# Optimization experiments

Measured on AMD Instinct MI355X. Metric: run time of the kernel, lower is better.

Reference implementation:

```python
import jax, jax.numpy as jnp
import numpy as np

N_NODES = 100000
N_EDGES = 1600000
N_GRAPHS = 128
IN_FEATS = 128
OUT_FEATS = 64


def setup_inputs() -> dict:
    key = jax.random.key(0)
    k1, k2, k3, k4, k5, k6 = jax.random.split(key, 6)
    features = jax.random.normal(k1, (N_NODES, IN_FEATS), jnp.float32)
    src = jax.random.randint(k2, (N_EDGES,), 0, N_NODES, dtype=jnp.int32)
    dst = jax.random.randint(k3, (N_EDGES,), 0, N_NODES, dtype=jnp.int32)
    graph_ids = jnp.sort(jax.random.randint(k4, (N_NODES,), 0, N_GRAPHS, dtype=jnp.int32))
    # Xavier-uniform init as in DGL GraphConv
    lim1 = float(np.sqrt(6.0 / (IN_FEATS + IN_FEATS)))
    lim2 = float(np.sqrt(6.0 / (IN_FEATS + OUT_FEATS)))
    W1 = jax.random.uniform(k5, (IN_FEATS, IN_FEATS), jnp.float32, -lim1, lim1)
    W2 = jax.random.uniform(k6, (IN_FEATS, OUT_FEATS), jnp.float32, -lim2, lim2)
    b1 = jnp.zeros((IN_FEATS,), jnp.float32)
    b2 = jnp.zeros((OUT_FEATS,), jnp.float32)
    return {"features": features, "W1": W1, "b1": b1, "W2": W2, "b2": b2,
            "src": src, "dst": dst, "graph_ids": graph_ids, "num_graphs": N_GRAPHS}


def _graph_conv(x, W, b, src, dst, n_nodes):
    # DGL GraphConv, norm='both': D_dst^{-1/2} A D_src^{-1/2} X W + b
    ones = jnp.ones(src.shape, x.dtype)
    deg_out = jax.ops.segment_sum(ones, src, num_segments=n_nodes)
    deg_in = jax.ops.segment_sum(ones, dst, num_segments=n_nodes)
    norm_src = jax.lax.rsqrt(jnp.maximum(deg_out, 1.0))  # [N]
    norm_dst = jax.lax.rsqrt(jnp.maximum(deg_in, 1.0))   # [N]
    h = (x * norm_src[:, None]) @ W                       # dense transform first
    agg = jax.ops.segment_sum(h[src], dst, num_segments=n_nodes)  # spmm-style scatter-add
    return agg * norm_dst[:, None] + b


def reference(features, W1, b1, W2, b2, src, dst, graph_ids, num_graphs):
    n = features.shape[0]
    h = jax.nn.relu(_graph_conv(features, W1, b1, src, dst, n))
    h = jax.nn.relu(_graph_conv(h, W2, b2, src, dst, n))
    # dgl.mean_nodes: per-graph mean over nodes
    sums = jax.ops.segment_sum(h, graph_ids, num_segments=num_graphs)
    counts = jax.ops.segment_sum(jnp.ones((n, 1), h.dtype), graph_ids, num_segments=num_graphs)
    return sums / jnp.maximum(counts, 1.0)
```

## Files before the change

### kernel.cpp

```cpp
#include <hip/hip_runtime.h>
#include <hip/hip_bf16.h>


#define NPP_SHIFT 9
#define NPP 512
#define MAXP 256
#define NB 512
#define CAPP 10240

typedef __attribute__((ext_vector_type(8))) short frag8;
typedef __attribute__((ext_vector_type(4))) float f32x4;
typedef __attribute__((ext_vector_type(2))) float v2f;

__launch_bounds__(256)
__global__ void buildC(const int* __restrict__ src, const int* __restrict__ dst,
                       int E, int P, int* __restrict__ cur,
                       int2* __restrict__ ebuf_dst, int* __restrict__ deg,
                       const int* __restrict__ gids, int N, int G,
                       int* __restrict__ gcnt) {
    __shared__ int h[MAXP], bs[MAXP], hg[MAXP];
    int tid = threadIdx.x;
    for (int i = tid; i < MAXP; i += 256) { h[i] = 0; hg[i] = 0; }
    __syncthreads();
    int per_block = (E + NB - 1) / NB;
    int e0 = blockIdx.x * per_block;
    int e1 = min(e0 + per_block, E);
    for (int e = e0 + tid; e < e1; e += 256) {
        atomicAdd(&h[dst[e] >> NPP_SHIFT], 1);
        atomicAdd(&deg[src[e]], 1);
    }
    int npb = (N + NB - 1) / NB;
    int n0 = blockIdx.x * npb;
    int n1 = min(n0 + npb, N);
    for (int i = n0 + tid; i < n1; i += 256) atomicAdd(&hg[gids[i]], 1);
    __syncthreads();
    for (int p = tid; p < P; p += 256) {
        int c = h[p];
        bs[p] = c ? atomicAdd(&cur[p], c) : 0;
        h[p] = 0;
    }
    for (int i = tid; i < G; i += 256)
        if (hg[i]) atomicAdd(&gcnt[i], hg[i]);
    __syncthreads();
    for (int e = e0 + tid; e < e1; e += 256) {
        int d = dst[e];
        int s = src[e];
        int p = d >> NPP_SHIFT;
        int lp = atomicAdd(&h[p], 1);
        ebuf_dst[(size_t)p * CAPP + bs[p] + lp] = make_int2(d, s);
    }
}

__launch_bounds__(512)
__global__ void passD2(const int2* __restrict__ ebuf_dst, const int* __restrict__ cur,
                       int* __restrict__ row_start, int* __restrict__ csr_src,
                       int N, int E, int P) {
    __shared__ int hd[NPP], sc[NPP];
    int tid = threadIdx.x;
    int p = blockIdx.x;
    sc[tid] = (tid < P) ? cur[tid] : 0;
    __syncthreads();
    for (int off = 1; off < 512; off <<= 1) {
        int t = (tid >= off) ? sc[tid - off] : 0;
        __syncthreads();
        sc[tid] += t;
        __syncthreads();
    }
    int gbase = (p > 0) ? sc[p - 1] : 0;
    __syncthreads();
    int node_lo = p << NPP_SHIFT;
    int nl = min(NPP, N - node_lo);
    hd[tid] = 0;
    __syncthreads();
    int ndst = cur[p];
    size_t base_d = (size_t)p * CAPP;
    for (int i = tid; i < ndst; i += 512)
        atomicAdd(&hd[ebuf_dst[base_d + i].x - node_lo], 1);
    __syncthreads();
    int myh = hd[tid];
    sc[tid] = myh;
    __syncthreads();
    for (int off = 1; off < 512; off <<= 1) {
        int t = (tid >= off) ? sc[tid - off] : 0;
        __syncthreads();
        sc[tid] += t;
        __syncthreads();
    }
    int row0 = gbase + sc[tid] - myh;
    if (tid < nl) row_start[node_lo + tid] = row0;
    if (p == P - 1 && tid == 0) row_start[N] = E;
    __syncthreads();
    hd[tid] = row0;
    __syncthreads();
    for (int i = tid; i < ndst; i += 512) {
        int2 r = ebuf_dst[base_d + i];
        int pos = atomicAdd(&hd[r.x - node_lo], 1);
        csr_src[pos] = r.y;
    }
}

template <int COLS, bool BF16IN, bool PERM, bool FP8OUT>
__launch_bounds__(256)
__global__ void gemm_mfma(const void* __restrict__ xin, const float* __restrict__ w,
                          const int* __restrict__ deg,
                          void* __restrict__ out, int n) {
    constexpr int NT = COLS / 16;
    __shared__ short wlds[4 * NT * 64 * 8];
    const int tid = threadIdx.x;
    for (int i = tid; i < 128 * COLS / 4; i += 256) {
        int k = (i * 4) / COLS;
        int n0 = (i * 4) % COLS;
        float4 wv;
        if constexpr (PERM) {
            int ksrc = 64 * ((k >> 2) & 1) + 16 * (k & 3) + (k >> 3);
            wv = *reinterpret_cast<const float4*>(w + (size_t)ksrc * COLS + n0);
        } else {
            wv = reinterpret_cast<const float4*>(w)[i];
        }
        int c = k >> 5, q = (k >> 3) & 3, j = k & 7;
        float vals[4] = {wv.x, wv.y, wv.z, wv.w};
#pragma unroll
        for (int u = 0; u < 4; ++u) {
            int nn = n0 + u;
            int t = nn >> 4;
            int ln = (q << 4) | (nn & 15);
            union { __hip_bfloat16 b; short s; } cv;
            cv.b = __float2bfloat16(vals[u]);
            wlds[(((c * NT + t) << 6) | ln) * 8 + j] = cv.s;
        }
    }
    __syncthreads();

    const int lane = tid & 63;
    const int wid = tid >> 6;
    const int m = lane & 15;
    const int q = lane >> 4;
    const int ntiles = (n + 15) >> 4;
    const frag8* wfr = reinterpret_cast<const frag8*>(wlds);

    for (int wt = blockIdx.x * 4 + wid; wt < ntiles; wt += gridDim.x * 4) {
        const int row = (wt << 4) + m;
        frag8 af[4];
        if (row < n) {
            if constexpr (BF16IN) {
                const frag8* xp = reinterpret_cast<const frag8*>(
                    (const __hip_bfloat16*)xin + (size_t)row * 128);
#pragma unroll
                for (int c = 0; c < 4; ++c) af[c] = xp[c * 4 + q];
            } else {
                const float* xp = (const float*)xin + (size_t)row * 128;
                float nm = rsqrtf((float)max(deg[row], 1));
#pragma unroll
                for (int c = 0; c < 4; ++c) {
                    int base = c * 32 + q * 8;
                    float4 v0 = *reinterpret_cast<const float4*>(xp + base);
                    float4 v1 = *reinterpret_cast<const float4*>(xp + base + 4);
                    union { frag8 f; short s[8]; } a;
                    union { __hip_bfloat16 b; short s; } cv;
                    cv.b = __float2bfloat16(v0.x * nm); a.s[0] = cv.s;
                    cv.b = __float2bfloat16(v0.y * nm); a.s[1] = cv.s;
                    cv.b = __float2bfloat16(v0.z * nm); a.s[2] = cv.s;
                    cv.b = __float2bfloat16(v0.w * nm); a.s[3] = cv.s;
                    cv.b = __float2bfloat16(v1.x * nm); a.s[4] = cv.s;
                    cv.b = __float2bfloat16(v1.y * nm); a.s[5] = cv.s;
                    cv.b = __float2bfloat16(v1.z * nm); a.s[6] = cv.s;
                    cv.b = __float2bfloat16(v1.w * nm); a.s[7] = cv.s;
                    af[c] = a.f;
                }
            }
        } else {
#pragma unroll
            for (int c = 0; c < 4; ++c) af[c] = frag8{0, 0, 0, 0, 0, 0, 0, 0};
        }
        f32x4 acc[NT] = {};
#pragma unroll
        for (int c = 0; c < 4; ++c)
#pragma unroll
            for (int t = 0; t < NT; ++t)
                acc[t] = __builtin_amdgcn_mfma_f32_16x16x32_bf16(
                    af[c], wfr[(c * NT + t) * 64 + lane], acc[t], 0, 0, 0);
#pragma unroll
        for (int r = 0; r < 4; ++r) {
            int grow = (wt << 4) + q * 4 + r;
            if (grow < n) {
                if constexpr (FP8OUT && COLS == 128) {
                    uint w0 = 0, w1 = 0;
                    w0 = (uint)__builtin_amdgcn_cvt_pk_fp8_f32(acc[0][r], acc[1][r], (int)w0, false);
                    w0 = (uint)__builtin_amdgcn_cvt_pk_fp8_f32(acc[2][r], acc[3][r], (int)w0, true);
                    w1 = (uint)__builtin_amdgcn_cvt_pk_fp8_f32(acc[4][r], acc[5][r], (int)w1, false);
                    w1 = (uint)__builtin_amdgcn_cvt_pk_fp8_f32(acc[6][r], acc[7][r], (int)w1, true);
                    reinterpret_cast<uint2*>(out)[(size_t)grow * 16 + m] = make_uint2(w0, w1);
                } else if constexpr (FP8OUT) {
                    uint w0 = 0;
                    w0 = (uint)__builtin_amdgcn_cvt_pk_fp8_f32(acc[0][r], acc[1][r], (int)w0, false);
                    w0 = (uint)__builtin_amdgcn_cvt_pk_fp8_f32(acc[2][r], acc[3][r], (int)w0, true);
                    reinterpret_cast<uint*>(out)[(size_t)grow * 16 + m] = w0;
                } else {
                    __hip_bfloat16* ob = reinterpret_cast<__hip_bfloat16*>(out);
#pragma unroll
                    for (int t = 0; t < NT; ++t)
                        ob[(size_t)grow * COLS + t * 16 + m] = __float2bfloat16(acc[t][r]);
                }
            }
        }
    }
}

__launch_bounds__(256)
__global__ void spmm1_kernel(const uint2* __restrict__ h1,
                             const int* __restrict__ row_start,
                             const int* __restrict__ csr_src,
                             const float* __restrict__ b1,
                             const int* __restrict__ deg,
                             uint4* __restrict__ x2n, int n) {
    int wv = (blockIdx.x * blockDim.x + threadIdx.x) >> 6;
    int lane = threadIdx.x & 63;
    int r0 = wv * 2;
    if (r0 >= n) return;
    int a = lane >> 4;
    int s = lane & 15;
    int e0[2], e1[2];
#pragma unroll
    for (int r = 0; r < 2; ++r) {
        int rr = min(r0 + r, n - 1);
        e0[r] = row_start[rr];
        e1[r] = row_start[rr + 1];
        if (r0 + r >= n) e1[r] = e0[r];
    }
    v2f acc[2][4] = {};
    int nb = max((e1[0] - e0[0] + 15) >> 4, (e1[1] - e0[1] + 15) >> 4);
    for (int b = 0; b < nb; ++b) {
        uint2 v[2][4];
#pragma unroll
        for (int r = 0; r < 2; ++r) {
            int base = e0[r] + b * 16;
            if (base + 16 <= e1[r]) {
#pragma unroll
                for (int j = 0; j < 4; ++j)
                    v[r][j] = h1[(size_t)csr_src[base + 4 * j + a] * 16 + s];
            } else if (base < e1[r]) {
#pragma unroll
                for (int j = 0; j < 4; ++j) {
                    int idx = base + 4 * j + a;
                    int cidx = min(idx, e1[r] - 1);
                    uint2 vv = h1[(size_t)csr_src[cidx] * 16 + s];
                    bool ok = idx < e1[r];
                    v[r][j].x = ok ? vv.x : 0u;
                    v[r][j].y = ok ? vv.y : 0u;
                }
            } else {
#pragma unroll
                for (int j = 0; j < 4; ++j) v[r][j] = make_uint2(0u, 0u);
            }
        }
#pragma unroll
        for (int r = 0; r < 2; ++r)
#pragma unroll
            for (int j = 0; j < 4; ++j) {
                acc[r][0] += __builtin_amdgcn_cvt_pk_f32_fp8((int)v[r][j].x, false);
                acc[r][1] += __builtin_amdgcn_cvt_pk_f32_fp8((int)v[r][j].x, true);
                acc[r][2] += __builtin_amdgcn_cvt_pk_f32_fp8((int)v[r][j].y, false);
                acc[r][3] += __builtin_amdgcn_cvt_pk_f32_fp8((int)v[r][j].y, true);
            }
    }
#pragma unroll
    for (int r = 0; r < 2; ++r)
#pragma unroll
        for (int k = 0; k < 4; ++k) {
            v2f t;
            t[0] = __shfl_xor(acc[r][k][0], 16);
            t[1] = __shfl_xor(acc[r][k][1], 16);
            acc[r][k] += t;
            t[0] = __shfl_xor(acc[r][k][0], 32);
            t[1] = __shfl_xor(acc[r][k][1], 32);
            acc[r][k] += t;
        }
    if (a == 0) {
        float bbl[4] = {b1[s], b1[32 + s], b1[64 + s], b1[96 + s]};
        float bbh[4] = {b1[16 + s], b1[48 + s], b1[80 + s], b1[112 + s]};
#pragma unroll
        for (int r = 0; r < 2; ++r) {
            if (r0 + r < n) {
                float nd = rsqrtf((float)max(e1[r] - e0[r], 1));
                float ns = rsqrtf((float)max(deg[r0 + r], 1));
                uint w[4];
#pragma unroll
                for (int k = 0; k < 4; ++k) {
                    float fl = fmaxf(fmaf(acc[r][k][0], nd, bbl[k]), 0.f) * ns;
                    float fh = fmaxf(fmaf(acc[r][k][1], nd, bbh[k]), 0.f) * ns;
                    union { __hip_bfloat16 b; ushort u; } cl, ch;
                    cl.b = __float2bfloat16(fl);
                    ch.b = __float2bfloat16(fh);
                    w[k] = (uint)cl.u | ((uint)ch.u << 16);
                }
                x2n[(size_t)(r0 + r) * 16 + s] = make_uint4(w[0], w[1], w[2], w[3]);
            }
        }
    }
}

__launch_bounds__(256)
__global__ void spmm2_kernel(const uint* __restrict__ h2,
                             const int* __restrict__ row_start,
                             const int* __restrict__ csr_src,
                             const float* __restrict__ b2,
                             const int* __restrict__ gids,
                             const int* __restrict__ gcnt,
                             float* __restrict__ out, int n) {
    int wv = (blockIdx.x * blockDim.x + threadIdx.x) >> 6;
    int lane = threadIdx.x & 63;
    int wave = threadIdx.x >> 6;
    int r0 = wv * 4;
    int a = lane >> 4;
    int s = lane & 15;
    int e0[4], e1[4], g[4];
    float inv[4];
#pragma unroll
    for (int r = 0; r < 4; ++r) {
        int rr = min(r0 + r, n - 1);
        e0[r] = row_start[rr];
        e1[r] = row_start[rr + 1];
        g[r] = gids[rr];
        if (r0 + r >= n) { e1[r] = e0[r]; g[r] = -1; }
        inv[r] = 1.f / (float)max(gcnt[max(g[r], 0)], 1);
    }
    float acc[4][4] = {};
    int nb = 0;
#pragma unroll
    for (int r = 0; r < 4; ++r) nb = max(nb, (e1[r] - e0[r] + 15) >> 4);
    for (int b = 0; b < nb; ++b) {
        uint u[4][4];
#pragma unroll
        for (int r = 0; r < 4; ++r) {
            int base = e0[r] + b * 16;
            if (base + 16 <= e1[r]) {
#pragma unroll
                for (int j = 0; j < 4; ++j)
                    u[r][j] = h2[(size_t)csr_src[base + 4 * j + a] * 16 + s];
            } else if (base < e1[r]) {
#pragma unroll
                for (int j = 0; j < 4; ++j) {
                    int idx = base + 4 * j + a;
                    int cidx = min(idx, e1[r] - 1);
                    uint vv = h2[(size_t)csr_src[cidx] * 16 + s];
                    u[r][j] = (idx < e1[r]) ? vv : 0u;
                }
            } else {
#pragma unroll
                for (int j = 0; j < 4; ++j) u[r][j] = 0u;
            }
        }
#pragma unroll
        for (int r = 0; r < 4; ++r)
#pragma unroll
            for (int j = 0; j < 4; ++j) {
                v2f lo = __builtin_amdgcn_cvt_pk_f32_fp8((int)u[r][j], false);
                v2f hi = __builtin_amdgcn_cvt_pk_f32_fp8((int)u[r][j], true);
                acc[r][0] += lo[0]; acc[r][1] += lo[1];
                acc[r][2] += hi[0]; acc[r][3] += hi[1];
            }
    }
#pragma unroll
    for (int r = 0; r < 4; ++r)
#pragma unroll
        for (int k = 0; k < 4; ++k) {
            acc[r][k] += __shfl_xor(acc[r][k], 16);
            acc[r][k] += __shfl_xor(acc[r][k], 32);
        }
    float bb0 = b2[s], bb1 = b2[16 + s], bb2v = b2[32 + s], bb3 = b2[48 + s];
    float val[4][4];
#pragma unroll
    for (int r = 0; r < 4; ++r) {
        float nd = rsqrtf((float)max(e1[r] - e0[r], 1));
        bool vld = g[r] >= 0;
        val[r][0] = vld ? fmaxf(fmaf(acc[r][0], nd, bb0), 0.f) * inv[r] : 0.f;
        val[r][1] = vld ? fmaxf(fmaf(acc[r][1], nd, bb1), 0.f) * inv[r] : 0.f;
        val[r][2] = vld ? fmaxf(fmaf(acc[r][2], nd, bb2v), 0.f) * inv[r] : 0.f;
        val[r][3] = vld ? fmaxf(fmaf(acc[r][3], nd, bb3), 0.f) * inv[r] : 0.f;
    }
    __shared__ float sbuf[4][64];
    __shared__ int sg[4];
    bool same = (g[0] == g[1]) && (g[1] == g[2]) && (g[2] == g[3]) && (g[0] >= 0);
    int sgw;
    if (same) {
        if (a == 0) {
            sbuf[wave][s]      = val[0][0] + val[1][0] + val[2][0] + val[3][0];
            sbuf[wave][16 + s] = val[0][1] + val[1][1] + val[2][1] + val[3][1];
            sbuf[wave][32 + s] = val[0][2] + val[1][2] + val[2][2] + val[3][2];
            sbuf[wave][48 + s] = val[0][3] + val[1][3] + val[2][3] + val[3][3];
        }
        sgw = g[0];
    } else {
        if (a == 0) {
#pragma unroll
            for (int r = 0; r < 4; ++r) {
                if (g[r] >= 0) {
                    atomicAdd(&out[(size_t)g[r] * 64 + s], val[r][0]);
                    atomicAdd(&out[(size_t)g[r] * 64 + 16 + s], val[r][1]);
                    atomicAdd(&out[(size_t)g[r] * 64 + 32 + s], val[r][2]);
                    atomicAdd(&out[(size_t)g[r] * 64 + 48 + s], val[r][3]);
                }
            }
            sbuf[wave][s] = 0.f;
            sbuf[wave][16 + s] = 0.f;
            sbuf[wave][32 + s] = 0.f;
            sbuf[wave][48 + s] = 0.f;
        }
        sgw = -1;
    }
    if (lane == 0) sg[wave] = sgw;
    __syncthreads();
    if (wave == 0) {
        int g0 = sg[0], g1 = sg[1], g2 = sg[2], g3 = sg[3];
        if (g0 == g1 && g1 == g2 && g2 == g3 && g0 >= 0) {
            float ssum = sbuf[0][lane] + sbuf[1][lane] + sbuf[2][lane] + sbuf[3][lane];
            atomicAdd(&out[(size_t)g0 * 64 + lane], ssum);
        } else {
#pragma unroll
            for (int w = 0; w < 4; ++w)
                if (sg[w] >= 0)
                    atomicAdd(&out[(size_t)sg[w] * 64 + lane], sbuf[w][lane]);
        }
    }
}

extern "C" void kernel_launch(void* const* d_in, const int* in_sizes, int n_in,
                              void* d_out, int out_size, void* d_ws, size_t ws_size,
                              hipStream_t stream) {
    const float* features = (const float*)d_in[0];
    const float* W1 = (const float*)d_in[1];
    const float* b1 = (const float*)d_in[2];
    const float* W2 = (const float*)d_in[3];
    const float* b2 = (const float*)d_in[4];
    const int* src = (const int*)d_in[5];
    const int* dst = (const int*)d_in[6];
    const int* gids = (const int*)d_in[7];
    const int N = in_sizes[7];
    const int E = in_sizes[5];
    const int G = out_size / 64;
    float* out = (float*)d_out;
    const int P = (N + NPP - 1) >> NPP_SHIFT;

    char* ws = (char*)d_ws;
    size_t off = 0;
    auto alloc = [&](size_t bytes) -> void* {
        void* p = ws + off;
        off = (off + bytes + 255) & ~(size_t)255;
        return p;
    };
    int* zblock = (int*)alloc((size_t)(G + N + P) * 4);
    int* gcnt = zblock;
    int* deg = zblock + G;
    int* cur = deg + N;
    int2* ebuf_dst = (int2*)alloc((size_t)P * CAPP * 8);
    int* row_start = (int*)alloc((size_t)(N + 1) * 4);
    int* csr_src = (int*)alloc((size_t)E * 4);
    uint* h1 = (uint*)alloc((size_t)N * 128);
    __hip_bfloat16* x2n = (__hip_bfloat16*)alloc((size_t)N * 128 * 2);
    uint* h2 = h1;

    hipMemsetAsync(out, 0, (size_t)out_size * sizeof(float), stream);
    hipMemsetAsync(zblock, 0, (size_t)(G + N + P) * 4, stream);

    buildC<<<NB, 256, 0, stream>>>(src, dst, E, P, cur, ebuf_dst, deg, gids, N, G, gcnt);
    passD2<<<P, 512, 0, stream>>>(ebuf_dst, cur, row_start, csr_src, N, E, P);

    gemm_mfma<128, false, false, true><<<768, 256, 0, stream>>>(features, W1, deg,
                                                                (void*)h1, N);
    {
        int waves = (N + 1) / 2;
        int blocks = (waves * 64 + 255) / 256;
        spmm1_kernel<<<blocks, 256, 0, stream>>>((const uint2*)h1, row_start, csr_src, b1,
                                                 deg, (uint4*)x2n, N);
    }
    gemm_mfma<64, true, true, true><<<768, 256, 0, stream>>>(x2n, W2, nullptr,
                                                             (void*)h2, N);
    {
        int waves = (N + 3) / 4;
        int blocks = (waves * 64 + 255) / 256;
        spmm2_kernel<<<blocks, 256, 0, stream>>>(h2, row_start, csr_src, b2,
                                                 gids, gcnt, out, N);
    }
}
```

Before: 318.7 us.

## Replace global out-degree atomics with partitioned src buckets and shared-memory counting

Out-degree is no longer computed with 1.6M random global atomicAdds on deg[src]. Source ids are now bucketed by node partition into a new ebuf_src buffer, and passD3 counts them with shared-memory atomics, writing norm_src directly as a precomputed rsqrt. The GEMM and spmm1 then read the float norm instead of recomputing it from deg. This adds an extra 6.4MB scatter write and a read-back pass in exchange for removing contended global atomics.

New measurement: 285.0 us (median of 2 runs). -10.6%, faster.

```diff
diff --git a/kernel.cpp b/kernel.cpp
--- a/kernel.cpp
+++ b/kernel.cpp
@@ -13,21 +13,21 @@
 typedef __attribute__((ext_vector_type(2))) float v2f;
 
 __launch_bounds__(256)
-__global__ void buildC(const int* __restrict__ src, const int* __restrict__ dst,
-                       int E, int P, int* __restrict__ cur,
-                       int2* __restrict__ ebuf_dst, int* __restrict__ deg,
-                       const int* __restrict__ gids, int N, int G,
-                       int* __restrict__ gcnt) {
-    __shared__ int h[MAXP], bs[MAXP], hg[MAXP];
+__global__ void buildAC(const int* __restrict__ src, const int* __restrict__ dst,
+                        int E, int P, int* __restrict__ cur,
+                        int* __restrict__ ebuf_src, int2* __restrict__ ebuf_dst,
+                        const int* __restrict__ gids, int N, int G,
+                        int* __restrict__ gcnt) {
+    __shared__ int hs[MAXP], hd[MAXP], bs1[MAXP], bs2[MAXP], hg[MAXP];
     int tid = threadIdx.x;
-    for (int i = tid; i < MAXP; i += 256) { h[i] = 0; hg[i] = 0; }
+    for (int i = tid; i < MAXP; i += 256) { hs[i] = 0; hd[i] = 0; hg[i] = 0; }
     __syncthreads();
     int per_block = (E + NB - 1) / NB;
     int e0 = blockIdx.x * per_block;
     int e1 = min(e0 + per_block, E);
     for (int e = e0 + tid; e < e1; e += 256) {
-        atomicAdd(&h[dst[e] >> NPP_SHIFT], 1);
-        atomicAdd(&deg[src[e]], 1);
+        atomicAdd(&hs[src[e] >> NPP_SHIFT], 1);
+        atomicAdd(&hd[dst[e] >> NPP_SHIFT], 1);
     }
     int npb = (N + NB - 1) / NB;
     int n0 = blockIdx.x * npb;
@@ -35,30 +35,37 @@
     for (int i = n0 + tid; i < n1; i += 256) atomicAdd(&hg[gids[i]], 1);
     __syncthreads();
     for (int p = tid; p < P; p += 256) {
-        int c = h[p];
-        bs[p] = c ? atomicAdd(&cur[p], c) : 0;
-        h[p] = 0;
+        int c1 = hs[p];
+        bs1[p] = c1 ? atomicAdd(&cur[p], c1) : 0;
+        int c2 = hd[p];
+        bs2[p] = c2 ? atomicAdd(&cur[P + p], c2) : 0;
+        hs[p] = 0;
+        hd[p] = 0;
     }
     for (int i = tid; i < G; i += 256)
         if (hg[i]) atomicAdd(&gcnt[i], hg[i]);
     __syncthreads();
     for (int e = e0 + tid; e < e1; e += 256) {
+        int s = src[e];
         int d = dst[e];
-        int s = src[e];
-        int p = d >> NPP_SHIFT;
-        int lp = atomicAdd(&h[p], 1);
-        ebuf_dst[(size_t)p * CAPP + bs[p] + lp] = make_int2(d, s);
+        int p1 = s >> NPP_SHIFT;
+        int p2 = d >> NPP_SHIFT;
+        int l1 = atomicAdd(&hs[p1], 1);
+        ebuf_src[(size_t)p1 * CAPP + bs1[p1] + l1] = s;
+        int l2 = atomicAdd(&hd[p2], 1);
+        ebuf_dst[(size_t)p2 * CAPP + bs2[p2] + l2] = make_int2(d, s);
     }
 }
 
 __launch_bounds__(512)
-__global__ void passD2(const int2* __restrict__ ebuf_dst, const int* __restrict__ cur,
+__global__ void passD3(const int* __restrict__ ebuf_src, const int2* __restrict__ ebuf_dst,
+                       const int* __restrict__ cur, float* __restrict__ norm_src,
                        int* __restrict__ row_start, int* __restrict__ csr_src,
                        int N, int E, int P) {
-    __shared__ int hd[NPP], sc[NPP];
+    __shared__ int hs[NPP], hd[NPP], sc[NPP];
     int tid = threadIdx.x;
     int p = blockIdx.x;
-    sc[tid] = (tid < P) ? cur[tid] : 0;
+    sc[tid] = (tid < P) ? cur[P + tid] : 0;
     __syncthreads();
     for (int off = 1; off < 512; off <<= 1) {
         int t = (tid >= off) ? sc[tid - off] : 0;
@@ -70,13 +77,19 @@
     __syncthreads();
     int node_lo = p << NPP_SHIFT;
     int nl = min(NPP, N - node_lo);
+    hs[tid] = 0;
     hd[tid] = 0;
     __syncthreads();
-    int ndst = cur[p];
+    int nsrc = cur[p];
+    size_t base_s = (size_t)p * CAPP;
+    for (int i = tid; i < nsrc; i += 512)
+        atomicAdd(&hs[ebuf_src[base_s + i] - node_lo], 1);
+    int ndst = cur[P + p];
     size_t base_d = (size_t)p * CAPP;
     for (int i = tid; i < ndst; i += 512)
         atomicAdd(&hd[ebuf_dst[base_d + i].x - node_lo], 1);
     __syncthreads();
+    if (tid < nl) norm_src[node_lo + tid] = rsqrtf((float)max(hs[tid], 1));
     int myh = hd[tid];
     sc[tid] = myh;
     __syncthreads();
@@ -102,7 +115,7 @@
 template <int COLS, bool BF16IN, bool PERM, bool FP8OUT>
 __launch_bounds__(256)
 __global__ void gemm_mfma(const void* __restrict__ xin, const float* __restrict__ w,
-                          const int* __restrict__ deg,
+                          const float* __restrict__ norm,
                           void* __restrict__ out, int n) {
     constexpr int NT = COLS / 16;
     __shared__ short wlds[4 * NT * 64 * 8];
@@ -149,7 +162,7 @@
                 for (int c = 0; c < 4; ++c) af[c] = xp[c * 4 + q];
             } else {
                 const float* xp = (const float*)xin + (size_t)row * 128;
-                float nm = rsqrtf((float)max(deg[row], 1));
+                float nm = norm[row];
 #pragma unroll
                 for (int c = 0; c < 4; ++c) {
                     int base = c * 32 + q * 8;
@@ -211,7 +224,7 @@
                              const int* __restrict__ row_start,
                              const int* __restrict__ csr_src,
                              const float* __restrict__ b1,
-                             const int* __restrict__ deg,
+                             const float* __restrict__ norm_src,
                              uint4* __restrict__ x2n, int n) {
     int wv = (blockIdx.x * blockDim.x + threadIdx.x) >> 6;
     int lane = threadIdx.x & 63;
@@ -282,7 +295,7 @@
         for (int r = 0; r < 2; ++r) {
             if (r0 + r < n) {
                 float nd = rsqrtf((float)max(e1[r] - e0[r], 1));
-                float ns = rsqrtf((float)max(deg[r0 + r], 1));
+                float ns = norm_src[r0 + r];
                 uint w[4];
 #pragma unroll
                 for (int k = 0; k < 4; ++k) {
@@ -448,11 +461,12 @@
         off = (off + bytes + 255) & ~(size_t)255;
         return p;
     };
-    int* zblock = (int*)alloc((size_t)(G + N + P) * 4);
+    int* zblock = (int*)alloc((size_t)(G + 2 * P) * 4);
     int* gcnt = zblock;
-    int* deg = zblock + G;
-    int* cur = deg + N;
+    int* cur = zblock + G;
+    int* ebuf_src = (int*)alloc((size_t)P * CAPP * 4);
     int2* ebuf_dst = (int2*)alloc((size_t)P * CAPP * 8);
+    float* norm_src = (float*)alloc((size_t)N * 4);
     int* row_start = (int*)alloc((size_t)(N + 1) * 4);
     int* csr_src = (int*)alloc((size_t)E * 4);
     uint* h1 = (uint*)alloc((size_t)N * 128);
@@ -460,18 +474,20 @@
     uint* h2 = h1;
 
     hipMemsetAsync(out, 0, (size_t)out_size * sizeof(float), stream);
-    hipMemsetAsync(zblock, 0, (size_t)(G + N + P) * 4, stream);
-
-    buildC<<<NB, 256, 0, stream>>>(src, dst, E, P, cur, ebuf_dst, deg, gids, N, G, gcnt);
-    passD2<<<P, 512, 0, stream>>>(ebuf_dst, cur, row_start, csr_src, N, E, P);
-
-    gemm_mfma<128, false, false, true><<<768, 256, 0, stream>>>(features, W1, deg,
+    hipMemsetAsync(zblock, 0, (size_t)(G + 2 * P) * 4, stream);
+
+    buildAC<<<NB, 256, 0, stream>>>(src, dst, E, P, cur, ebuf_src, ebuf_dst,
+                                    gids, N, G, gcnt);
+    passD3<<<P, 512, 0, stream>>>(ebuf_src, ebuf_dst, cur, norm_src, row_start,
+                                  csr_src, N, E, P);
+
+    gemm_mfma<128, false, false, true><<<768, 256, 0, stream>>>(features, W1, norm_src,
                                                                 (void*)h1, N);
     {
         int waves = (N + 1) / 2;
         int blocks = (waves * 64 + 255) / 256;
         spmm1_kernel<<<blocks, 256, 0, stream>>>((const uint2*)h1, row_start, csr_src, b1,
-                                                 deg, (uint4*)x2n, N);
+                                                 norm_src, (uint4*)x2n, N);
     }
     gemm_mfma<64, true, true, true><<<768, 256, 0, stream>>>(x2n, W2, nullptr,
                                                              (void*)h2, N);
```
